# Kernel optimization log

Measured on AMD Instinct MI355X. Metric: run time of the kernel, lower is better.

## Reference

```python
import jax, jax.numpy as jnp
import numpy as np

OUT = 7           # pooled output size
SR = 2            # sampling_ratio
SCALES = (0.25, 0.125, 0.0625, 0.03125)
K_MIN = 2         # -log2(scales[0])
CANON_SCALE = 224.0
CANON_LVL = 4.0
EPS = 1e-6


def map_levels(boxes):
    # boxes: [N,4] in image coords -> level index in [0, 3]
    area = (boxes[:, 2] - boxes[:, 0]) * (boxes[:, 3] - boxes[:, 1])
    s = jnp.sqrt(area)
    lvl = jnp.floor(CANON_LVL + jnp.log2(s / CANON_SCALE + EPS))
    lvl = jnp.clip(lvl, K_MIN, K_MIN + len(SCALES) - 1)
    return lvl.astype(jnp.int32) - K_MIN


def _sample_coords(lo, bin_sz):
    # sample points within each of OUT bins, SR samples per bin -> [OUT*SR]
    grid = (jnp.arange(OUT, dtype=jnp.float32)[:, None] * bin_sz
            + (jnp.arange(SR, dtype=jnp.float32)[None, :] + 0.5) * bin_sz / SR)
    return lo + grid.reshape(-1)


def _roi_align_single(feat, img, box, scale):
    # feat: [B,C,H,W] (closed over batch under vmap), img: scalar int, box: [4]
    H, W = feat.shape[2], feat.shape[3]
    x1 = box[0] * scale
    y1 = box[1] * scale
    x2 = box[2] * scale
    y2 = box[3] * scale
    roi_w = jnp.maximum(x2 - x1, 1.0)
    roi_h = jnp.maximum(y2 - y1, 1.0)
    ys = _sample_coords(y1, roi_h / OUT)  # [14]
    xs = _sample_coords(x1, roi_w / OUT)  # [14]
    P = OUT * SR
    yg = jnp.broadcast_to(ys[:, None], (P, P)).reshape(-1)  # [196]
    xg = jnp.broadcast_to(xs[None, :], (P, P)).reshape(-1)  # [196]
    # ROIAlign CUDA semantics: out-of-range samples contribute 0
    valid = (yg >= -1.0) & (yg <= H) & (xg >= -1.0) & (xg <= W)
    y = jnp.clip(yg, 0.0, H - 1)
    x = jnp.clip(xg, 0.0, W - 1)
    y0 = jnp.floor(y).astype(jnp.int32)
    x0 = jnp.floor(x).astype(jnp.int32)
    y1i = jnp.minimum(y0 + 1, H - 1)
    x1i = jnp.minimum(x0 + 1, W - 1)
    ly = y - y0
    lx = x - x0
    hy = 1.0 - ly
    hx = 1.0 - lx
    # advanced indices (img, y, x) separated by ':' slice -> result [196, C]
    v00 = feat[img, :, y0, x0]
    v01 = feat[img, :, y0, x1i]
    v10 = feat[img, :, y1i, x0]
    v11 = feat[img, :, y1i, x1i]
    val = ((hy * hx)[:, None] * v00 + (hy * lx)[:, None] * v01
           + (ly * hx)[:, None] * v10 + (ly * lx)[:, None] * v11)
    val = jnp.where(valid[:, None], val, 0.0)
    # [196,C] -> [OUT,SR,OUT,SR,C] -> average over sampling grid -> [OUT,OUT,C]
    val = val.reshape(OUT, SR, OUT, SR, -1).mean(axis=(1, 3))
    return jnp.transpose(val, (2, 0, 1))  # [C,7,7]


def _pooler(feats, boxes, img_ids):
    levels = map_levels(boxes)  # [N]
    N = boxes.shape[0]
    C = feats[0].shape[1]
    result = jnp.zeros((N, C, OUT, OUT), dtype=feats[0].dtype)
    roi_align = jax.vmap(_roi_align_single, in_axes=(None, 0, 0, None))
    for lvl, (feat, scale) in enumerate(zip(feats, SCALES)):
        out_l = roi_align(feat, img_ids, boxes, scale)  # [N,C,7,7]
        result = jnp.where((levels == lvl)[:, None, None, None], out_l, result)
    return result


def setup_inputs() -> dict:
    key = jax.random.key(0)
    ks = jax.random.split(key, 7)
    B, C, N = 2, 256, 1000
    feat0 = jax.random.normal(ks[0], (B, C, 200, 200), jnp.float32)
    feat1 = jax.random.normal(ks[1], (B, C, 100, 100), jnp.float32)
    feat2 = jax.random.normal(ks[2], (B, C, 50, 50), jnp.float32)
    feat3 = jax.random.normal(ks[3], (B, C, 25, 25), jnp.float32)
    # log-uniform box sizes in [16, 400] px spread ROIs across all 4 levels
    wh = jnp.exp(jax.random.uniform(ks[4], (N, 2), minval=jnp.log(16.0),
                                    maxval=jnp.log(400.0)))
    xy = jax.random.uniform(ks[5], (N, 2)) * (800.0 - wh)
    boxes = jnp.concatenate([xy, xy + wh], axis=1)  # [N,4] x1,y1,x2,y2
    img_ids = jax.random.randint(ks[6], (N,), 0, B, dtype=jnp.int32)
    return {"feat0": feat0, "feat1": feat1, "feat2": feat2, "feat3": feat3,
            "boxes": boxes, "img_ids": img_ids}


def reference(feat0, feat1, feat2, feat3, boxes, img_ids):
    return _pooler((feat0, feat1, feat2, feat3), boxes, img_ids)
```

## Files before the change

kernel.cpp:

```cpp
#include <hip/hip_runtime.h>

#define OUTD 7
#define SRD 2
#define PD (OUTD * SRD)
#define NCH 256
#define CHUNK 64

__global__ __launch_bounds__(256)
void pooler_kernel(const float* __restrict__ f0,
                   const float* __restrict__ f1,
                   const float* __restrict__ f2,
                   const float* __restrict__ f3,
                   const float* __restrict__ boxes,
                   const int*   __restrict__ img_ids,
                   float* __restrict__ out)
{
    const int roi = blockIdx.x;
    const int c0  = blockIdx.y * CHUNK;
    const int t   = threadIdx.x;

    const float bx1 = boxes[roi * 4 + 0];
    const float by1 = boxes[roi * 4 + 1];
    const float bx2 = boxes[roi * 4 + 2];
    const float by2 = boxes[roi * 4 + 3];

    const float area = (bx2 - bx1) * (by2 - by1);
    const float s    = sqrtf(area);
    float lvlf = floorf(4.0f + log2f(s / 224.0f + 1e-6f));
    lvlf = fminf(fmaxf(lvlf, 2.0f), 5.0f);
    const int lvl = (int)lvlf - 2;

    const float scales[4] = {0.25f, 0.125f, 0.0625f, 0.03125f};
    const int   dims[4]   = {200, 100, 50, 25};
    const float* feats[4] = {f0, f1, f2, f3};

    const float scale = scales[lvl];
    const int H = dims[lvl];
    const int W = H;
    const int plane = H * W;

    const int img = img_ids[roi];
    const float* __restrict__ base0 =
        feats[lvl] + (size_t)img * NCH * (size_t)plane + (size_t)c0 * plane;

    const float x1 = bx1 * scale, y1 = by1 * scale;
    const float x2 = bx2 * scale, y2 = by2 * scale;
    const float roi_w = fmaxf(x2 - x1, 1.0f);
    const float roi_h = fmaxf(y2 - y1, 1.0f);
    const float bw = roi_w / (float)OUTD;
    const float bh = roi_h / (float)OUTD;

    __shared__ float4 s_yt[PD];
    __shared__ float4 s_xt[PD];
    __shared__ float4 s_xw[OUTD];
    __shared__ int    s_xf[OUTD];
    __shared__ int    s_ok[OUTD];

    if (t < PD) {
        const int i = t >> 1, j = t & 1;
        const float yg = y1 + (float)i * bh + ((float)j + 0.5f) * bh * 0.5f;
        const float v = ((yg >= -1.0f) && (yg <= (float)H)) ? 1.0f : 0.0f;
        const float y = fminf(fmaxf(yg, 0.0f), (float)(H - 1));
        const int y0 = (int)floorf(y);
        const int y1i = min(y0 + 1, H - 1);
        const float ly = y - (float)y0;
        float4 r;
        r.x = __int_as_float(y0 * W);
        r.y = __int_as_float(y1i * W);
        r.z = (1.0f - ly) * v;
        r.w = ly * v;
        s_yt[t] = r;
    } else if (t < 2 * PD) {
        const int tt = t - PD;
        const int i = tt >> 1, j = tt & 1;
        const float xg = x1 + (float)i * bw + ((float)j + 0.5f) * bw * 0.5f;
        const float v = ((xg >= -1.0f) && (xg <= (float)W)) ? 1.0f : 0.0f;
        const float x = fminf(fmaxf(xg, 0.0f), (float)(W - 1));
        const int x0 = (int)floorf(x);
        const float lx = x - (float)x0;
        const float hx = 1.0f - lx;
        const int edge = (x0 == W - 1);
        float4 r;
        r.x = __int_as_float(min(x0, W - 2));
        r.y = edge ? 0.0f   : hx * v;
        r.z = edge ? hx * v : lx * v;
        r.w = 0.0f;
        s_xt[tt] = r;
    } else if (t < 2 * PD + OUTD) {
        const int pw = t - 2 * PD;
        float w[4] = {0.0f, 0.0f, 0.0f, 0.0f};
        int ca[2], cb[2];
        float hxv[2], lxv[2];
#pragma unroll
        for (int j = 0; j < 2; ++j) {
            const float xg = x1 + (float)pw * bw + ((float)j + 0.5f) * bw * 0.5f;
            const float v = ((xg >= -1.0f) && (xg <= (float)W)) ? 1.0f : 0.0f;
            const float x = fminf(fmaxf(xg, 0.0f), (float)(W - 1));
            const int x0 = (int)floorf(x);
            const float lx = x - (float)x0;
            ca[j] = x0;
            cb[j] = min(x0 + 1, W - 1);
            hxv[j] = (1.0f - lx) * v;
            lxv[j] = lx * v;
        }
        const int ok = (cb[1] - ca[0]) <= 3;
        int xf = min(ca[0], W - 4);
        if (xf < 0) xf = 0;
        w[(ca[0] - xf) & 3] += hxv[0];
        w[(cb[0] - xf) & 3] += lxv[0];
        w[(ca[1] - xf) & 3] += hxv[1];
        w[(cb[1] - xf) & 3] += lxv[1];
        float4 wv; wv.x = w[0]; wv.y = w[1]; wv.z = w[2]; wv.w = w[3];
        s_xw[pw] = wv;
        s_xf[pw] = xf;
        s_ok[pw] = ok;
    }
    __syncthreads();

    const bool fused = s_ok[0] && s_ok[1] && s_ok[2] && s_ok[3] &&
                       s_ok[4] && s_ok[5] && s_ok[6];

    float* __restrict__ outbase = out + ((size_t)roi * NCH + c0) * 49;

    if (fused) {
        auto g4 = [&](const float* __restrict__ fp, int ph, int pw, float4* P) {
            const float4 yt0 = s_yt[2 * ph];
            const float4 yt1 = s_yt[2 * ph + 1];
            const int xf = s_xf[pw];
            P[0] = *(const float4*)(fp + __float_as_int(yt0.x) + xf);
            P[1] = *(const float4*)(fp + __float_as_int(yt0.y) + xf);
            P[2] = *(const float4*)(fp + __float_as_int(yt1.x) + xf);
            P[3] = *(const float4*)(fp + __float_as_int(yt1.y) + xf);
        };
        auto r4 = [&](int ph, int pw, const float4* P) -> float {
            const float4 w   = s_xw[pw];
            const float4 yt0 = s_yt[2 * ph];
            const float4 yt1 = s_yt[2 * ph + 1];
            const float d0 = w.x * P[0].x + w.y * P[0].y + w.z * P[0].z + w.w * P[0].w;
            const float d1 = w.x * P[1].x + w.y * P[1].y + w.z * P[1].z + w.w * P[1].w;
            const float d2 = w.x * P[2].x + w.y * P[2].y + w.z * P[2].z + w.w * P[2].w;
            const float d3 = w.x * P[3].x + w.y * P[3].y + w.z * P[3].z + w.w * P[3].w;
            return yt0.z * d0 + yt0.w * d1 + yt1.z * d2 + yt1.w * d3;
        };

        int e0 = t;
#pragma unroll
        for (int kk = 0; kk < 4; ++kk) {
            const int ea = e0, eb = e0 + 256, ec = e0 + 512;
            e0 += 768;
            const int cA = ea / 49, binA = ea - cA * 49;
            const int phA = binA / 7, pwA = binA - phA * 7;
            const int cB = eb / 49, binB = eb - cB * 49;
            const int phB = binB / 7, pwB = binB - phB * 7;
            const int cC = ec / 49, binC = ec - cC * 49;
            const int phC = binC / 7, pwC = binC - phC * 7;

            const float* fa = base0 + (size_t)cA * plane;
            const float* fb = base0 + (size_t)cB * plane;
            const float* fc = base0 + (size_t)cC * plane;

            float4 PA[4], PB[4], PC[4];
            g4(fa, phA, pwA, PA);
            g4(fb, phB, pwB, PB);
            g4(fc, phC, pwC, PC);

            outbase[ea] = r4(phA, pwA, PA) * 0.25f;
            outbase[eb] = r4(phB, pwB, PB) * 0.25f;
            outbase[ec] = r4(phC, pwC, PC) * 0.25f;
        }
        if (t < 64) {
            const int e = 3072 + t;
            const int c = e / 49, bin = e - c * 49;
            const int ph = bin / 7, pw = bin - ph * 7;
            const float* fp = base0 + (size_t)c * plane;
            float4 P[4];
            g4(fp, ph, pw, P);
            outbase[e] = r4(ph, pw, P) * 0.25f;
        }
    } else {
        auto gather = [&](const float* __restrict__ fp, int ph, int pw, float2* P) {
#pragma unroll
            for (int sy = 0; sy < SRD; ++sy) {
                const float4 yt = s_yt[ph * SRD + sy];
                const int ro0 = __float_as_int(yt.x);
                const int ro1 = __float_as_int(yt.y);
#pragma unroll
                for (int sx = 0; sx < SRD; ++sx) {
                    const float4 xt = s_xt[pw * SRD + sx];
                    const int xa = __float_as_int(xt.x);
                    P[(sy * SRD + sx) * 2 + 0] = *(const float2*)(fp + ro0 + xa);
                    P[(sy * SRD + sx) * 2 + 1] = *(const float2*)(fp + ro1 + xa);
                }
            }
        };
        auto reduce = [&](int ph, int pw, const float2* P) -> float {
            float acc = 0.0f;
#pragma unroll
            for (int sy = 0; sy < SRD; ++sy) {
                const float4 yt = s_yt[ph * SRD + sy];
                const float hy = yt.z, ly = yt.w;
#pragma unroll
                for (int sx = 0; sx < SRD; ++sx) {
                    const float4 xt = s_xt[pw * SRD + sx];
                    const float wlo = xt.y, whi = xt.z;
                    const float2 p0 = P[(sy * SRD + sx) * 2 + 0];
                    const float2 p1 = P[(sy * SRD + sx) * 2 + 1];
                    acc += hy * (wlo * p0.x + whi * p0.y)
                         + ly * (wlo * p1.x + whi * p1.y);
                }
            }
            return acc;
        };

        int e0 = t;
#pragma unroll
        for (int kk = 0; kk < 6; ++kk) {
            const int ea = e0;
            const int eb = e0 + 256;
            e0 += 512;

            const int ca = ea / 49, bina = ea - ca * 49;
            const int pha = bina / 7, pwa = bina - pha * 7;
            const int cb = eb / 49, binb = eb - cb * 49;
            const int phb = binb / 7, pwb = binb - phb * 7;

            const float* fa = base0 + (size_t)ca * plane;
            const float* fb = base0 + (size_t)cb * plane;

            float2 PA[8], PB[8];
            gather(fa, pha, pwa, PA);
            gather(fb, phb, pwb, PB);

            outbase[ea] = reduce(pha, pwa, PA) * 0.25f;
            outbase[eb] = reduce(phb, pwb, PB) * 0.25f;
        }
        if (t < 64) {
            const int e = 12 * 256 + t;
            const int c = e / 49, bin = e - c * 49;
            const int ph = bin / 7, pw = bin - ph * 7;
            const float* fp = base0 + (size_t)c * plane;
            float2 P[8];
            gather(fp, ph, pw, P);
            outbase[e] = reduce(ph, pw, P) * 0.25f;
        }
    }
}

extern "C" void kernel_launch(void* const* d_in, const int* in_sizes, int n_in,
                              void* d_out, int out_size, void* d_ws, size_t ws_size,
                              hipStream_t stream) {
    const float* f0    = (const float*)d_in[0];
    const float* f1    = (const float*)d_in[1];
    const float* f2    = (const float*)d_in[2];
    const float* f3    = (const float*)d_in[3];
    const float* boxes = (const float*)d_in[4];
    const int*   ids   = (const int*)d_in[5];
    float* out = (float*)d_out;

    const int N = in_sizes[4] / 4;

    dim3 grid(N, NCH / CHUNK);
    pooler_kernel<<<grid, 256, 0, stream>>>(f0, f1, f2, f3, boxes, ids, out);
}
```

Before: 234.2 us.

## Sort ROIs by level, image and Morton center to improve cache locality

Adds a single-block bitonic sort kernel that orders ROIs by pyramid level, image id and a Morton code of the box center. The pooler then processes ROIs in that order, with block indices swizzled by 8 so that ROIs with nearby centers land on the same XCD-like group of blocks. The aim is to raise L2 hit rates for the bilinear gathers. The cost is an extra kernel launch, a serial 1024-element sort on one block, and a hard limit of N<=1024.

```diff
diff --git a/kernel.cpp b/kernel.cpp
--- a/kernel.cpp
+++ b/kernel.cpp
@@ -5,6 +5,54 @@
 #define PD (OUTD * SRD)
 #define NCH 256
 #define CHUNK 64
+
+__global__ __launch_bounds__(1024)
+void sort_kernel(const float* __restrict__ boxes,
+                 const int*   __restrict__ img_ids,
+                 int* __restrict__ order, int N)
+{
+    __shared__ unsigned long long kv[1024];
+    const int t = threadIdx.x;
+
+    unsigned int key = 0xFFFFFFFFu;
+    if (t < N) {
+        const float bx1 = boxes[t * 4 + 0];
+        const float by1 = boxes[t * 4 + 1];
+        const float bx2 = boxes[t * 4 + 2];
+        const float by2 = boxes[t * 4 + 3];
+        const float area = (bx2 - bx1) * (by2 - by1);
+        const float s = sqrtf(area);
+        float lvlf = floorf(4.0f + log2f(s / 224.0f + 1e-6f));
+        lvlf = fminf(fmaxf(lvlf, 2.0f), 5.0f);
+        const int lvl = (int)lvlf - 2;
+        const float scales[4] = {0.25f, 0.125f, 0.0625f, 0.03125f};
+        const float sc = scales[lvl];
+        int cx = (int)(0.5f * (bx1 + bx2) * sc);
+        int cy = (int)(0.5f * (by1 + by2) * sc);
+        cx = min(max(cx, 0), 127);
+        cy = min(max(cy, 0), 127);
+        unsigned int m = 0;
+#pragma unroll
+        for (int b = 0; b < 7; ++b)
+            m |= ((cy >> b) & 1u) << (2 * b + 1) | ((cx >> b) & 1u) << (2 * b);
+        key = ((((unsigned)lvl << 1) | (unsigned)img_ids[t]) << 14) | m;
+    }
+    kv[t] = ((unsigned long long)key << 32) | (unsigned)t;
+    __syncthreads();
+
+    for (int k = 2; k <= 1024; k <<= 1) {
+        for (int j = k >> 1; j > 0; j >>= 1) {
+            const int ixj = t ^ j;
+            if (ixj > t) {
+                const bool up = ((t & k) == 0);
+                const unsigned long long a = kv[t], b = kv[ixj];
+                if ((a > b) == up) { kv[t] = b; kv[ixj] = a; }
+            }
+            __syncthreads();
+        }
+    }
+    if (t < N) order[t] = (int)(kv[t] & 0xFFFFFFFFu);
+}
 
 __global__ __launch_bounds__(256)
 void pooler_kernel(const float* __restrict__ f0,
@@ -13,9 +61,18 @@
                    const float* __restrict__ f3,
                    const float* __restrict__ boxes,
                    const int*   __restrict__ img_ids,
-                   float* __restrict__ out)
+                   const int*   __restrict__ order,
+                   float* __restrict__ out, int N)
 {
-    const int roi = blockIdx.x;
+    int bx = blockIdx.x;
+    int sidx;
+    if ((N & 7) == 0) {
+        sidx = (bx & 7) * (N >> 3) + (bx >> 3);
+    } else {
+        sidx = bx;
+    }
+    const int roi = order[sidx];
+
     const int c0  = blockIdx.y * CHUNK;
     const int t   = threadIdx.x;
 
@@ -256,9 +313,12 @@
     const float* boxes = (const float*)d_in[4];
     const int*   ids   = (const int*)d_in[5];
     float* out = (float*)d_out;
+    int*   order = (int*)d_ws;
 
     const int N = in_sizes[4] / 4;
 
+    sort_kernel<<<1, 1024, 0, stream>>>(boxes, ids, order, N);
+
     dim3 grid(N, NCH / CHUNK);
-    pooler_kernel<<<grid, 256, 0, stream>>>(f0, f1, f2, f3, boxes, ids, out);
+    pooler_kernel<<<grid, 256, 0, stream>>>(f0, f1, f2, f3, boxes, ids, order, out, N);
 }
```

New measurement: 233.3 us. About the same (-0.4%).
